# Optimization experiments

Hardware: AMD Instinct MI355X
Metric: run time of the kernel (lower is better)

The kernel has to match this reference:

```python
import jax, jax.numpy as jnp
import numpy as np

FIELD_DIMS = 100000
FACTORS = 16
BATCH = 1024


def setup_inputs() -> dict:
    key = jax.random.key(0)
    k1, k2 = jax.random.split(key)
    # multi-hot indicator rows (values in {0,1}); row>0 selects active embedding rows
    x0 = jax.random.randint(k1, (BATCH, FIELD_DIMS), 0, 2, dtype=jnp.int32)
    # embedding table (truncated_normal init in the original; plain normal scaled is fine for a numeric reference)
    W = jax.random.normal(k2, (FIELD_DIMS, FACTORS), dtype=jnp.float32) * 0.05
    return {"x0": x0, "W": W}


def reference(x0, W):
    # Original per-row math: let E = W[row > 0] (active embedding rows)
    #   out = 0.5 * ( sum_{i,j} e_i . e_j  -  sum_i ||e_i||^2 )
    # sum_{i,j} e_i . e_j == || sum_i e_i ||^2, so with multi-hot mask m:
    #   s  = m @ W                     -> [B, k]
    #   q  = m @ rowwise_sumsq(W)      -> [B]
    #   out = 0.5 * (||s||^2 - q)      -> [B]
    m = (x0 > 0).astype(W.dtype)                    # [B, F]
    s = m @ W                                        # [B, k]
    q = m @ jnp.sum(W * W, axis=-1)                  # [B]
    return 0.5 * (jnp.sum(s * s, axis=-1) - q)
```

## Files before the change

kernel.cpp:

```cpp
#include <hip/hip_runtime.h>

#define FIELDS  100000
#define FACTORS 16
#define BATCH   1024
#define BT      8
#define NCHUNK  8
#define FPC     (FIELDS / NCHUNK)
#define BLOCK   256
#define TF      512
#define NTF     (FPC / TF)
#define TAILPG  ((FPC - NTF * TF) / 4)
#define NBUF    2

typedef __attribute__((address_space(1))) const void gvoid;
typedef __attribute__((address_space(3))) void lvoid;

__global__ __launch_bounds__(BLOCK, 4) void fm_partial(
    const int* __restrict__ x0, const float* __restrict__ W,
    float* __restrict__ ws)
{
    __shared__ __align__(16) int xbuf[NBUF][BT][TF];
    __shared__ float red[4][BT][17];

    const int t     = threadIdx.x;
    const int bid   = blockIdx.x;
    const int rg    = bid >> 3;
    const int chunk = bid & (NCHUNK - 1);
    const int b0    = rg * BT;
    const int fbeg  = chunk * FPC;

    const int qr   = t & 3;
    const int pg   = t >> 2;
    const int lane = t & 63;
    const int wv   = t >> 6;

    float acc[BT][4], qac[BT];
#pragma unroll
    for (int r = 0; r < BT; ++r) {
        qac[r] = 0.f;
#pragma unroll
        for (int j = 0; j < 4; ++j) acc[r][j] = 0.f;
    }

    const char* x0b = (const char*)x0;
    const char* Wb  = (const char*)W;

    const int r0 = 2 * wv, r1 = r0 + 1;
    const unsigned sb0 = ((unsigned)(b0 + r0) * FIELDS + (unsigned)fbeg) * 4u
                       + (unsigned)lane * 16u;
    const unsigned sb1 = sb0 + FIELDS * 4u;
    char* const l0 = (char*)&xbuf[0][r0][0] + lane * 16;
    char* const l1 = (char*)&xbuf[0][r1][0] + lane * 16;

#define STAGE(buf, tile) do {                                               \
        const unsigned _so = (unsigned)(tile) * (TF * 4u);                  \
        __builtin_amdgcn_global_load_lds((gvoid*)(x0b + (sb0 + _so)),       \
            (lvoid*)(l0 + (buf) * (BT * TF * 4)), 16, 0, 0);                \
        __builtin_amdgcn_global_load_lds((gvoid*)(x0b + (sb0 + _so + 1024u)),\
            (lvoid*)(l0 + (buf) * (BT * TF * 4) + 1024), 16, 0, 0);         \
        __builtin_amdgcn_global_load_lds((gvoid*)(x0b + (sb1 + _so)),       \
            (lvoid*)(l1 + (buf) * (BT * TF * 4)), 16, 0, 0);                \
        __builtin_amdgcn_global_load_lds((gvoid*)(x0b + (sb1 + _so + 1024u)),\
            (lvoid*)(l1 + (buf) * (BT * TF * 4) + 1024), 16, 0, 0);         \
    } while (0)

#define FMTILE(p0, p1, p2, p3, BUFEXPR)                                     \
    do {                                                                    \
        const float s0 = fmaf(p0.x, p0.x, fmaf(p0.y, p0.y, fmaf(p0.z, p0.z, p0.w * p0.w))); \
        const float s1 = fmaf(p1.x, p1.x, fmaf(p1.y, p1.y, fmaf(p1.z, p1.z, p1.w * p1.w))); \
        const float s2 = fmaf(p2.x, p2.x, fmaf(p2.y, p2.y, fmaf(p2.z, p2.z, p2.w * p2.w))); \
        const float s3 = fmaf(p3.x, p3.x, fmaf(p3.y, p3.y, fmaf(p3.z, p3.z, p3.w * p3.w))); \
        _Pragma("unroll")                                                   \
        for (int r = 0; r < BT; ++r) {                                      \
            const int4 xv = BUFEXPR;                                        \
            const float m0 = (float)xv.x, m1 = (float)xv.y;                 \
            const float m2 = (float)xv.z, m3 = (float)xv.w;                 \
            qac[r]    = fmaf(m0, s0,   fmaf(m1, s1,   fmaf(m2, s2,   fmaf(m3, s3,   qac[r])))); \
            acc[r][0] = fmaf(m0, p0.x, fmaf(m1, p1.x, fmaf(m2, p2.x, fmaf(m3, p3.x, acc[r][0])))); \
            acc[r][1] = fmaf(m0, p0.y, fmaf(m1, p1.y, fmaf(m2, p2.y, fmaf(m3, p3.y, acc[r][1])))); \
            acc[r][2] = fmaf(m0, p0.z, fmaf(m1, p1.z, fmaf(m2, p2.z, fmaf(m3, p3.z, acc[r][2])))); \
            acc[r][3] = fmaf(m0, p0.w, fmaf(m1, p1.w, fmaf(m2, p2.w, fmaf(m3, p3.w, acc[r][3])))); \
        }                                                                   \
    } while (0)

    const unsigned wq = (unsigned)qr * 16u;
    const unsigned wbase = (unsigned)(fbeg + pg * 4) * 64u + wq;

    STAGE(0, 0);

#pragma unroll 1
    for (int tl = 0; tl < NTF; ++tl) {
        const unsigned wB = wbase + (unsigned)tl * (TF * 64u);
        const float4 wa0 = *(const float4*)(Wb + wB);
        const float4 wa1 = *(const float4*)(Wb + wB + 64u);
        const float4 wa2 = *(const float4*)(Wb + wB + 128u);
        const float4 wa3 = *(const float4*)(Wb + wB + 192u);
        const float4 wb0 = *(const float4*)(Wb + wB + 16384u);
        const float4 wb1 = *(const float4*)(Wb + wB + 16384u + 64u);
        const float4 wb2 = *(const float4*)(Wb + wB + 16384u + 128u);
        const float4 wb3 = *(const float4*)(Wb + wB + 16384u + 192u);

        asm volatile("s_waitcnt vmcnt(8)" ::: "memory");
        __builtin_amdgcn_s_barrier();
        __builtin_amdgcn_sched_barrier(0);

        if (tl + 1 < NTF) STAGE((tl + 1) & 1, tl + 1);
        __builtin_amdgcn_sched_barrier(0);

        const int buf = tl & 1;
        FMTILE(wa0, wa1, wa2, wa3, (*(const int4*)&xbuf[buf][r][pg * 4]));
        FMTILE(wb0, wb1, wb2, wb3, (*(const int4*)&xbuf[buf][r][256 + pg * 4]));
    }

    {
        const bool valid = (pg < TAILPG);
        const int  pgc   = valid ? pg : (TAILPG - 1);
        const unsigned fb = (unsigned)(fbeg + NTF * TF + pgc * 4);
        const unsigned wT = fb * 64u + wq;
        float4 w0 = *(const float4*)(Wb + wT);
        float4 w1 = *(const float4*)(Wb + wT + 64u);
        float4 w2 = *(const float4*)(Wb + wT + 128u);
        float4 w3 = *(const float4*)(Wb + wT + 192u);
        if (!valid) {
            w0.x=w0.y=w0.z=w0.w=0.f; w1.x=w1.y=w1.z=w1.w=0.f;
            w2.x=w2.y=w2.z=w2.w=0.f; w3.x=w3.y=w3.z=w3.w=0.f;
        }
        FMTILE(w0, w1, w2, w3,
               (*(const int4*)(x0b + ((unsigned)(b0 + r) * FIELDS + fb) * 4u)));
    }

#pragma unroll
    for (int r = 0; r < BT; ++r) {
#pragma unroll
        for (int off = 4; off < 64; off <<= 1) {
            acc[r][0] += __shfl_xor(acc[r][0], off);
            acc[r][1] += __shfl_xor(acc[r][1], off);
            acc[r][2] += __shfl_xor(acc[r][2], off);
            acc[r][3] += __shfl_xor(acc[r][3], off);
        }
#pragma unroll
        for (int off = 1; off < 64; off <<= 1)
            qac[r] += __shfl_xor(qac[r], off);
    }

    if (lane < 4) {
#pragma unroll
        for (int r = 0; r < BT; ++r) {
#pragma unroll
            for (int j = 0; j < 4; ++j)
                red[wv][r][lane * 4 + j] = acc[r][j];
            if (lane == 0) red[wv][r][16] = qac[r];
        }
    }
    __syncthreads();
    if (t < BT * 17) {
        const int r = t / 17;
        const int j = t % 17;
        const float v = red[0][r][j] + red[1][r][j] + red[2][r][j] + red[3][r][j];
        ws[((size_t)(b0 + r) * NCHUNK + chunk) * 17 + j] = v;
    }
#undef STAGE
#undef FMTILE
}

__global__ __launch_bounds__(BLOCK) void fm_final(
    const float* __restrict__ ws, float* __restrict__ out)
{
    const int b = blockIdx.x * BLOCK + threadIdx.x;
    if (b < BATCH) {
        const float* pbase = ws + (size_t)b * NCHUNK * 17;
        float s[17];
#pragma unroll
        for (int j = 0; j < 17; ++j) s[j] = 0.f;
#pragma unroll
        for (int c = 0; c < NCHUNK; ++c)
#pragma unroll
            for (int j = 0; j < 17; ++j) s[j] += pbase[c * 17 + j];
        float ss = 0.f;
#pragma unroll
        for (int k = 0; k < FACTORS; ++k) ss += s[k] * s[k];
        out[b] = 0.5f * (ss - s[16]);
    }
}

extern "C" void kernel_launch(void* const* d_in, const int* in_sizes, int n_in,
                              void* d_out, int out_size, void* d_ws, size_t ws_size,
                              hipStream_t stream)
{
    const int*   x0 = (const int*)d_in[0];
    const float* W  = (const float*)d_in[1];
    float* out = (float*)d_out;
    float* ws  = (float*)d_ws;

    fm_partial<<<dim3((BATCH / BT) * NCHUNK), dim3(BLOCK), 0, stream>>>(x0, W, ws);
    fm_final<<<dim3((BATCH + BLOCK - 1) / BLOCK), dim3(BLOCK), 0, stream>>>(ws, out);
}
```

Before: 111.7 us.

## Pack multi-hot mask into LDS bitmask via wave ballots before compute

Each block now reads its whole x0 chunk up front and compresses the int32 indicators into a bitmask in shared memory using wave ballots and bit-spreading, in place of double-buffered direct-to-LDS tiles of raw ints. The compute loop then reads one 32-bit word per row and extracts mask bits, which shrinks LDS footprint and LDS read traffic. The cost is that the x0 streaming no longer overlaps with the FMA work: the load phase and compute phase are serialized behind a barrier, and extra ALU work goes into packing and unpacking bits.

```diff
diff --git a/kernel.cpp b/kernel.cpp
--- a/kernel.cpp
+++ b/kernel.cpp
@@ -7,19 +7,24 @@
 #define NCHUNK  8
 #define FPC     (FIELDS / NCHUNK)
 #define BLOCK   256
+#define NSPANF  48
+#define WPR     392
 #define TF      512
 #define NTF     (FPC / TF)
 #define TAILPG  ((FPC - NTF * TF) / 4)
-#define NBUF    2
-
-typedef __attribute__((address_space(1))) const void gvoid;
-typedef __attribute__((address_space(3))) void lvoid;
+
+__device__ __forceinline__ unsigned spread8(unsigned x) {
+    x = (x | (x << 12)) & 0x000F000Fu;
+    x = (x | (x << 6))  & 0x03030303u;
+    x = (x | (x << 3))  & 0x11111111u;
+    return x;
+}
 
 __global__ __launch_bounds__(BLOCK, 4) void fm_partial(
     const int* __restrict__ x0, const float* __restrict__ W,
     float* __restrict__ ws)
 {
-    __shared__ __align__(16) int xbuf[NBUF][BT][TF];
+    __shared__ unsigned lmask[BT][WPR];
     __shared__ float red[4][BT][17];
 
     const int t     = threadIdx.x;
@@ -34,6 +39,51 @@
     const int lane = t & 63;
     const int wv   = t >> 6;
 
+    {
+        const int lr0 = 2 * wv, lr1 = lr0 + 1;
+        const int* xr0 = x0 + (size_t)(b0 + lr0) * FIELDS + fbeg;
+        const int* xr1 = x0 + (size_t)(b0 + lr1) * FIELDS + fbeg;
+        const int sh8 = 8 * (lane & 7);
+
+#define PACKW(xv, lrow, ss) do {                                            \
+        const unsigned long long B0 = __ballot((xv).x > 0);                 \
+        const unsigned long long B1 = __ballot((xv).y > 0);                 \
+        const unsigned long long B2 = __ballot((xv).z > 0);                 \
+        const unsigned long long B3 = __ballot((xv).w > 0);                 \
+        const unsigned word = spread8((unsigned)(B0 >> sh8) & 0xFFu)        \
+                      | (spread8((unsigned)(B1 >> sh8) & 0xFFu) << 1)       \
+                      | (spread8((unsigned)(B2 >> sh8) & 0xFFu) << 2)       \
+                      | (spread8((unsigned)(B3 >> sh8) & 0xFFu) << 3);      \
+        if (lane < 8) lmask[lrow][(ss) * 8 + lane] = word;                  \
+    } while (0)
+
+#pragma unroll 1
+        for (int s = 0; s < NSPANF; s += 4) {
+            int4 va[4], vb[4];
+#pragma unroll
+            for (int i = 0; i < 4; ++i) {
+                va[i] = *(const int4*)(xr0 + (s + i) * 256 + lane * 4);
+                vb[i] = *(const int4*)(xr1 + (s + i) * 256 + lane * 4);
+            }
+#pragma unroll
+            for (int i = 0; i < 4; ++i) {
+                PACKW(va[i], lr0, s + i);
+                PACKW(vb[i], lr1, s + i);
+            }
+        }
+        {
+            const bool v  = (lane < 53);
+            const int off = 12288 + (v ? lane * 4 : 0);
+            int4 xa = *(const int4*)(xr0 + off);
+            int4 xb = *(const int4*)(xr1 + off);
+            if (!v) { xa.x = xa.y = xa.z = xa.w = 0; xb.x = xb.y = xb.z = xb.w = 0; }
+            PACKW(xa, lr0, NSPANF);
+            PACKW(xb, lr1, NSPANF);
+        }
+#undef PACKW
+    }
+    __syncthreads();
+
     float acc[BT][4], qac[BT];
 #pragma unroll
     for (int r = 0; r < BT; ++r) {
@@ -42,29 +92,13 @@
         for (int j = 0; j < 4; ++j) acc[r][j] = 0.f;
     }
 
-    const char* x0b = (const char*)x0;
-    const char* Wb  = (const char*)W;
-
-    const int r0 = 2 * wv, r1 = r0 + 1;
-    const unsigned sb0 = ((unsigned)(b0 + r0) * FIELDS + (unsigned)fbeg) * 4u
-                       + (unsigned)lane * 16u;
-    const unsigned sb1 = sb0 + FIELDS * 4u;
-    char* const l0 = (char*)&xbuf[0][r0][0] + lane * 16;
-    char* const l1 = (char*)&xbuf[0][r1][0] + lane * 16;
-
-#define STAGE(buf, tile) do {                                               \
-        const unsigned _so = (unsigned)(tile) * (TF * 4u);                  \
-        __builtin_amdgcn_global_load_lds((gvoid*)(x0b + (sb0 + _so)),       \
-            (lvoid*)(l0 + (buf) * (BT * TF * 4)), 16, 0, 0);                \
-        __builtin_amdgcn_global_load_lds((gvoid*)(x0b + (sb0 + _so + 1024u)),\
-            (lvoid*)(l0 + (buf) * (BT * TF * 4) + 1024), 16, 0, 0);         \
-        __builtin_amdgcn_global_load_lds((gvoid*)(x0b + (sb1 + _so)),       \
-            (lvoid*)(l1 + (buf) * (BT * TF * 4)), 16, 0, 0);                \
-        __builtin_amdgcn_global_load_lds((gvoid*)(x0b + (sb1 + _so + 1024u)),\
-            (lvoid*)(l1 + (buf) * (BT * TF * 4) + 1024), 16, 0, 0);         \
-    } while (0)
-
-#define FMTILE(p0, p1, p2, p3, BUFEXPR)                                     \
+    const char* Wb = (const char*)W;
+    const unsigned wq    = (unsigned)qr * 16u;
+    const unsigned wbase = (unsigned)(fbeg + pg * 4) * 64u + wq;
+    const int pg8 = pg >> 3;
+    const int bb  = (pg * 4) & 31;
+
+#define FMHALF(p0, p1, p2, p3, WIDX)                                        \
     do {                                                                    \
         const float s0 = fmaf(p0.x, p0.x, fmaf(p0.y, p0.y, fmaf(p0.z, p0.z, p0.w * p0.w))); \
         const float s1 = fmaf(p1.x, p1.x, fmaf(p1.y, p1.y, fmaf(p1.z, p1.z, p1.w * p1.w))); \
@@ -72,9 +106,11 @@
         const float s3 = fmaf(p3.x, p3.x, fmaf(p3.y, p3.y, fmaf(p3.z, p3.z, p3.w * p3.w))); \
         _Pragma("unroll")                                                   \
         for (int r = 0; r < BT; ++r) {                                      \
-            const int4 xv = BUFEXPR;                                        \
-            const float m0 = (float)xv.x, m1 = (float)xv.y;                 \
-            const float m2 = (float)xv.z, m3 = (float)xv.w;                 \
+            const unsigned mw = lmask[r][WIDX];                             \
+            const float m0 = ((mw >> (bb + 0)) & 1u) ? 1.f : 0.f;           \
+            const float m1 = ((mw >> (bb + 1)) & 1u) ? 1.f : 0.f;           \
+            const float m2 = ((mw >> (bb + 2)) & 1u) ? 1.f : 0.f;           \
+            const float m3 = ((mw >> (bb + 3)) & 1u) ? 1.f : 0.f;           \
             qac[r]    = fmaf(m0, s0,   fmaf(m1, s1,   fmaf(m2, s2,   fmaf(m3, s3,   qac[r])))); \
             acc[r][0] = fmaf(m0, p0.x, fmaf(m1, p1.x, fmaf(m2, p2.x, fmaf(m3, p3.x, acc[r][0])))); \
             acc[r][1] = fmaf(m0, p0.y, fmaf(m1, p1.y, fmaf(m2, p2.y, fmaf(m3, p3.y, acc[r][1])))); \
@@ -82,11 +118,6 @@
             acc[r][3] = fmaf(m0, p0.w, fmaf(m1, p1.w, fmaf(m2, p2.w, fmaf(m3, p3.w, acc[r][3])))); \
         }                                                                   \
     } while (0)
-
-    const unsigned wq = (unsigned)qr * 16u;
-    const unsigned wbase = (unsigned)(fbeg + pg * 4) * 64u + wq;
-
-    STAGE(0, 0);
 
 #pragma unroll 1
     for (int tl = 0; tl < NTF; ++tl) {
@@ -99,17 +130,9 @@
         const float4 wb1 = *(const float4*)(Wb + wB + 16384u + 64u);
         const float4 wb2 = *(const float4*)(Wb + wB + 16384u + 128u);
         const float4 wb3 = *(const float4*)(Wb + wB + 16384u + 192u);
-
-        asm volatile("s_waitcnt vmcnt(8)" ::: "memory");
-        __builtin_amdgcn_s_barrier();
-        __builtin_amdgcn_sched_barrier(0);
-
-        if (tl + 1 < NTF) STAGE((tl + 1) & 1, tl + 1);
-        __builtin_amdgcn_sched_barrier(0);
-
-        const int buf = tl & 1;
-        FMTILE(wa0, wa1, wa2, wa3, (*(const int4*)&xbuf[buf][r][pg * 4]));
-        FMTILE(wb0, wb1, wb2, wb3, (*(const int4*)&xbuf[buf][r][256 + pg * 4]));
+        const int widx0 = tl * 16 + pg8;
+        FMHALF(wa0, wa1, wa2, wa3, widx0);
+        FMHALF(wb0, wb1, wb2, wb3, widx0 + 8);
     }
 
     {
@@ -125,9 +148,13 @@
             w0.x=w0.y=w0.z=w0.w=0.f; w1.x=w1.y=w1.z=w1.w=0.f;
             w2.x=w2.y=w2.z=w2.w=0.f; w3.x=w3.y=w3.z=w3.w=0.f;
         }
-        FMTILE(w0, w1, w2, w3,
-               (*(const int4*)(x0b + ((unsigned)(b0 + r) * FIELDS + fb) * 4u)));
-    }
+        const int widxT = NTF * 16 + (pgc >> 3);
+        const int bbT   = (pgc * 4) & 31;
+#define bb bbT
+        FMHALF(w0, w1, w2, w3, widxT);
+#undef bb
+    }
+#undef FMHALF
 
 #pragma unroll
     for (int r = 0; r < BT; ++r) {
@@ -159,8 +186,6 @@
         const float v = red[0][r][j] + red[1][r][j] + red[2][r][j] + red[3][r][j];
         ws[((size_t)(b0 + r) * NCHUNK + chunk) * 17 + j] = v;
     }
-#undef STAGE
-#undef FMTILE
 }
 
 __global__ __launch_bounds__(BLOCK) void fm_final(
```

Measured after the change: 194.9 us. 1.74x slower.
